# Optimization experiments

Hardware: AMD Instinct MI355X
Metric: run time of the kernel (lower is better)

## Reference

```python
import jax, jax.numpy as jnp
import numpy as np

GROUP_SIZE = 64
NUM_HEADS = 16
NUM_KV_HEADS = 4
ROPE_BASE = 10000.0


def rms_norm(x):
    eps = jnp.asarray(jnp.finfo(x.dtype).eps, x.dtype)
    return x * jax.lax.rsqrt(jnp.mean(x * x, axis=-1, keepdims=True) + eps)


def ternary_weight(w, g=GROUP_SIZE):
    # fake-quant with straight-through estimator, matching torch bf16 cast
    wb = w.astype(jnp.bfloat16)
    wg = wb.reshape(-1, g)
    scale = jnp.clip(jnp.mean(jnp.abs(wg), axis=-1, keepdims=True), 1e-8)
    q = jnp.clip(jnp.round(wg / scale), -1, 1)
    wq = (q * scale).reshape(w.shape)
    return wb + jax.lax.stop_gradient(wq - wb)


def ternary_linear(x, w):
    wt = ternary_weight(w).astype(x.dtype)
    return x @ wt.T


def apply_rotary_emb(x, cos, sin):
    half = x.shape[-1] // 2
    x1, x2 = x[..., :half], x[..., half:]
    return jnp.concatenate((x1 * cos + x2 * sin, x1 * -sin + x2 * cos), axis=-1)


def rotary_tables(seq_len, head_dim, dtype):
    inv_freq = 1.0 / (ROPE_BASE ** (jnp.arange(0, head_dim, 2, dtype=jnp.float32) / head_dim))
    freqs = jnp.outer(jnp.arange(seq_len, dtype=jnp.float32), inv_freq)  # [S, D/2]
    cos = jnp.cos(freqs)[None, :, None, :].astype(dtype)  # [1,S,1,D/2]
    sin = jnp.sin(freqs)[None, :, None, :].astype(dtype)
    return cos, sin


def setup_inputs() -> dict:
    key = jax.random.key(0)
    k1, k2, k3 = jax.random.split(key, 3)
    dim = 1024
    q_size = NUM_HEADS * (dim // NUM_HEADS)
    kv_size = NUM_KV_HEADS * (dim // NUM_HEADS)
    return {
        "x": jax.random.normal(k1, (2, 2048, dim), dtype=jnp.float32),
        "w_qkv": jax.random.normal(k2, (q_size + 2 * kv_size, dim), dtype=jnp.float32) * 0.02,
        "w_proj": jax.random.normal(k3, (dim, dim), dtype=jnp.float32) * 0.02,
        "q_gain": jnp.ones((NUM_HEADS,), dtype=jnp.float32),
    }


def reference(x, w_qkv, w_proj, q_gain):
    bsz, seqlen, dim = x.shape
    head_dim = dim // NUM_HEADS
    q_size = NUM_HEADS * head_dim
    kv_size = NUM_KV_HEADS * head_dim

    qkv = ternary_linear(x, w_qkv)
    q = qkv[..., :q_size].reshape(bsz, seqlen, NUM_HEADS, head_dim)
    k = qkv[..., q_size:q_size + kv_size].reshape(bsz, seqlen, NUM_KV_HEADS, head_dim)
    v = qkv[..., q_size + kv_size:].reshape(bsz, seqlen, NUM_KV_HEADS, head_dim)

    q, k = rms_norm(q), rms_norm(k)
    cos, sin = rotary_tables(seqlen, head_dim, q.dtype)
    q = apply_rotary_emb(q, cos, sin)
    k = apply_rotary_emb(k, cos, sin)
    q = q * q_gain.astype(q.dtype)[None, None, :, None]

    # GQA: repeat kv heads
    rep = NUM_HEADS // NUM_KV_HEADS
    kr = jnp.repeat(k, rep, axis=2)  # [B,S,H,D]
    vr = jnp.repeat(v, rep, axis=2)

    scale = 1.0 / jnp.sqrt(jnp.asarray(head_dim, q.dtype))
    scores = jnp.einsum('bqhd,bkhd->bhqk', q, kr) * scale  # [B,H,S,S]
    causal = jnp.tril(jnp.ones((seqlen, seqlen), dtype=bool))
    scores = jnp.where(causal[None, None], scores, jnp.asarray(-jnp.inf, scores.dtype))
    probs = jax.nn.softmax(scores, axis=-1)
    y = jnp.einsum('bhqk,bkhd->bqhd', probs, vr).reshape(bsz, seqlen, dim)

    # NormedTernaryLinear: rms_norm then ternary linear
    return ternary_linear(rms_norm(y), w_proj)
```

## Files before the change

kernel.cpp:

```cpp
#include <hip/hip_runtime.h>
#include <cstdint>

typedef unsigned short u16;
typedef __bf16 bf16x8 __attribute__((ext_vector_type(8)));
typedef __bf16 bf16x2 __attribute__((ext_vector_type(2)));
typedef short s16x4 __attribute__((ext_vector_type(4)));
typedef int s32x2 __attribute__((ext_vector_type(2)));
typedef float f32x4 __attribute__((ext_vector_type(4)));

__device__ __forceinline__ u16 f2bf(float f) {
    unsigned u = __float_as_uint(f);
    u = (u + 0x7fffu + ((u >> 16) & 1u)) >> 16;
    return (u16)u;
}
__device__ __forceinline__ float bf2f(u16 h) {
    return __uint_as_float(((unsigned)h) << 16);
}

__device__ __forceinline__ void glds16(const u16* g, u16* l) {
    __builtin_amdgcn_global_load_lds(
        (const __attribute__((address_space(1))) void*)g,
        (__attribute__((address_space(3))) void*)l, 16, 0, 0);
}

__device__ __forceinline__ s16x4 pack_bf4(float p0, float p1, float p2, float p3) {
    bf16x2 lo = {(__bf16)p0, (__bf16)p1};
    bf16x2 hi = {(__bf16)p2, (__bf16)p3};
    s32x2 pk = {__builtin_bit_cast(int, lo), __builtin_bit_cast(int, hi)};
    return __builtin_bit_cast(s16x4, pk);
}

#if __has_builtin(__builtin_amdgcn_mfma_f32_16x16x16bf16_1k)
#define MFMA16(a, b, c) __builtin_amdgcn_mfma_f32_16x16x16bf16_1k(a, b, c, 0, 0, 0)
#else
static __device__ __forceinline__ f32x4 mfma16_asm(s16x4 a, s16x4 b, f32x4 c) {
    asm("v_mfma_f32_16x16x16_bf16 %0, %1, %2, %0" : "+v"(c) : "v"(a), "v"(b));
    return c;
}
#define MFMA16(a, b, c) mfma16_asm(a, b, c)
#endif

__global__ __launch_bounds__(256) void prep(
    const float* __restrict__ w_qkv, const float* __restrict__ w_proj,
    const float* __restrict__ x,
    u16* __restrict__ wqkv_b, u16* __restrict__ wproj_b, u16* __restrict__ xb) {
    int bid = blockIdx.x;
    if (bid < 1280) {
        const float* w; u16* o; size_t base;
        if (bid < 768) { w = w_qkv; o = wqkv_b; base = (size_t)bid * 2048; }
        else { w = w_proj; o = wproj_b; base = (size_t)(bid - 768) * 2048; }
        size_t i = base + (size_t)threadIdx.x * 8;
        float4 A = *(const float4*)(w + i);
        float4 B = *(const float4*)(w + i + 4);
        float wf[8] = {A.x, A.y, A.z, A.w, B.x, B.y, B.z, B.w};
        float wbf[8], ab[8];
        #pragma unroll
        for (int e = 0; e < 8; ++e) { wbf[e] = bf2f(f2bf(wf[e])); ab[e] = fabsf(wbf[e]); }
        float s = ((ab[0] + ab[1]) + (ab[2] + ab[3])) + ((ab[4] + ab[5]) + (ab[6] + ab[7]));
        s += __shfl_xor(s, 1);
        s += __shfl_xor(s, 2);
        s += __shfl_xor(s, 4);
        float scale = bf2f(f2bf(s * (1.0f / 64.0f)));
        if (scale < 1e-8f) scale = 1e-8f;
        u16 ov[8];
        #pragma unroll
        for (int e = 0; e < 8; ++e) {
            float t = bf2f(f2bf(wbf[e] / scale));
            float q = rintf(t);
            q = fminf(1.0f, fmaxf(-1.0f, q));
            float d = bf2f(f2bf(q * scale - wbf[e]));
            ov[e] = f2bf(wbf[e] + d);
        }
        *(int4*)(o + i) = *(const int4*)ov;
    } else {
        size_t i = ((size_t)(bid - 1280) * 256 + threadIdx.x) * 8;
        float4 a = *(const float4*)(x + i);
        float4 b = *(const float4*)(x + i + 4);
        u16 o[8] = {f2bf(a.x), f2bf(a.y), f2bf(a.z), f2bf(a.w),
                    f2bf(b.x), f2bf(b.y), f2bf(b.z), f2bf(b.w)};
        *(int4*)(xb + i) = *(const int4*)o;
    }
}

__global__ __launch_bounds__(256) void gemm_qkv(
    const u16* __restrict__ A, const u16* __restrict__ B,
    const float* __restrict__ gain,
    u16* __restrict__ Qb, u16* __restrict__ Kb, u16* __restrict__ Vt) {
    __shared__ u16 As[2][128 * 32];
    __shared__ u16 Bs[2][64 * 32];
    const int tid = threadIdx.x;
    const int lane = tid & 63, w = tid >> 6;
    const int quad = lane >> 4, l16 = lane & 15;
    const int bx = blockIdx.x, by = blockIdx.y;
    const int n0 = bx * 64, t0 = by * 128;
    const bool vblk = bx >= 20;
    const int K = 1024, nk = 32;
    const int b = by >> 4;

    const int sra = w * 16 + (lane >> 2);
    const int srb = tid >> 2;
    const int sg4 = lane & 3;

    f32x4 acc[2][4];
    f32x4 zero = {0.f, 0.f, 0.f, 0.f};
    #pragma unroll
    for (int i = 0; i < 2; ++i)
        #pragma unroll
        for (int j = 0; j < 4; ++j) acc[i][j] = zero;

    int aoff[2], boff[4];
    #pragma unroll
    for (int mi = 0; mi < 2; ++mi) {
        int r = w * 32 + mi * 16 + l16;
        aoff[mi] = r * 32 + (quad ^ ((r >> 1) & 3)) * 8;
    }
    #pragma unroll
    for (int ni = 0; ni < 4; ++ni) {
        int rb = ni * 16 + l16;
        boff[ni] = rb * 32 + (quad ^ ((rb >> 1) & 3)) * 8;
    }

    #pragma unroll
    for (int i = 0; i < 2; ++i) {
        int r = sra + i * 64;
        int g = sg4 ^ ((r >> 1) & 3);
        glds16(A + (size_t)(t0 + r) * K + g * 8, &As[0][0] + (w * 16 + i * 64) * 32 + lane * 8);
    }
    {
        int g = sg4 ^ ((srb >> 1) & 3);
        glds16(B + (size_t)(n0 + srb) * K + g * 8, &Bs[0][0] + w * 512 + lane * 8);
    }
    __syncthreads();

    for (int kt = 0; kt < nk; ++kt) {
        if (kt + 1 < nk) {
            int k0 = (kt + 1) * 32, bi = (kt + 1) & 1;
            #pragma unroll
            for (int i = 0; i < 2; ++i) {
                int r = sra + i * 64;
                int g = sg4 ^ ((r >> 1) & 3);
                glds16(A + (size_t)(t0 + r) * K + k0 + g * 8, &As[bi][0] + (w * 16 + i * 64) * 32 + lane * 8);
            }
            int g = sg4 ^ ((srb >> 1) & 3);
            glds16(B + (size_t)(n0 + srb) * K + k0 + g * 8, &Bs[bi][0] + w * 512 + lane * 8);
        }
        const u16* as = &As[kt & 1][0];
        const u16* bs = &Bs[kt & 1][0];
        bf16x8 af[2], bfr[4];
        #pragma unroll
        for (int mi = 0; mi < 2; ++mi) af[mi]  = *(const bf16x8*)(as + aoff[mi]);
        #pragma unroll
        for (int ni = 0; ni < 4; ++ni) bfr[ni] = *(const bf16x8*)(bs + boff[ni]);
        if (!vblk) {
            #pragma unroll
            for (int mi = 0; mi < 2; ++mi)
                #pragma unroll
                for (int ni = 0; ni < 4; ++ni)
                    acc[mi][ni] = __builtin_amdgcn_mfma_f32_16x16x32_bf16(af[mi], bfr[ni], acc[mi][ni], 0, 0, 0);
        } else {
            #pragma unroll
            for (int mi = 0; mi < 2; ++mi)
                #pragma unroll
                for (int ni = 0; ni < 4; ++ni)
                    acc[mi][ni] = __builtin_amdgcn_mfma_f32_16x16x32_bf16(bfr[ni], af[mi], acc[mi][ni], 0, 0, 0);
        }
        __syncthreads();
    }

    if (vblk) {
        const int kv = bx - 20;
        u16* vbase = Vt + (size_t)(b * 4 + kv) * 64 * 2048;
        const int si = (t0 + w * 32 + l16) & 2047;
        #pragma unroll
        for (int mi = 0; mi < 2; ++mi)
            #pragma unroll
            for (int ni = 0; ni < 4; ++ni) {
                int d = ni * 16 + quad * 4;
                #pragma unroll
                for (int r = 0; r < 4; ++r)
                    vbase[(size_t)(d + r) * 2048 + si + mi * 16] = f2bf(acc[mi][ni][r]);
            }
    } else {
        const bool isQ = bx < 16;
        const float sc = 0.18033688011112042f;
        const float g = isQ ? gain[bx] * sc : 1.0f;
        u16* base = isQ ? (Qb + (size_t)(b * 16 + bx) * 2048 * 64)
                        : (Kb + (size_t)(b * 4 + (bx - 16)) * 2048 * 64);
        const float eps = 1.1920929e-7f;
        const float invf0 = (float)(1.0 / pow(10000.0, (double)l16 / 32.0));
        const float invf1 = (float)(1.0 / pow(10000.0, (double)(l16 + 16) / 32.0));
        #pragma unroll
        for (int mi = 0; mi < 2; ++mi) {
            #pragma unroll
            for (int r = 0; r < 4; ++r) {
                float v0 = acc[mi][0][r], v1 = acc[mi][1][r];
                float v2 = acc[mi][2][r], v3 = acc[mi][3][r];
                float ssq = (v0 * v0 + v1 * v1) + (v2 * v2 + v3 * v3);
                #pragma unroll
                for (int m = 1; m < 16; m <<= 1) ssq += __shfl_xor(ssq, m);
                float rn = 1.0f / sqrtf(ssq * (1.0f / 64.0f) + eps);
                int si = (t0 + w * 32 + mi * 16 + quad * 4 + r) & 2047;
                float a0 = (float)si * invf0, a1 = (float)si * invf1;
                float c0 = __cosf(a0), s0 = __sinf(a0);
                float c1 = __cosf(a1), s1 = __sinf(a1);
                float x1a = v0 * rn, x2a = v2 * rn;
                float x1b = v1 * rn, x2b = v3 * rn;
                u16* row = base + (size_t)si * 64;
                row[l16]      = f2bf((x1a * c0 + x2a * s0) * g);
                row[l16 + 32] = f2bf((x2a * c0 - x1a * s0) * g);
                row[l16 + 16] = f2bf((x1b * c1 + x2b * s1) * g);
                row[l16 + 48] = f2bf((x2b * c1 - x1b * s1) * g);
            }
        }
    }
}

__global__ __launch_bounds__(256) void gemm_bt(
    const u16* __restrict__ A, const u16* __restrict__ B,
    float* __restrict__ C, int M, int N, int K) {
    __shared__ u16 As[2][128 * 32];
    __shared__ u16 Bs[2][64 * 32];
    const int tid = threadIdx.x;
    const int lane = tid & 63, w = tid >> 6;
    const int quad = lane >> 4, l16 = lane & 15;
    const int m0 = blockIdx.y * 128, n0 = blockIdx.x * 64;
    const int wm = (w >> 1) * 64, wn = (w & 1) * 32;

    const int sra = w * 16 + (lane >> 2);
    const int srb = tid >> 2;
    const int sg4 = lane & 3;

    f32x4 acc[4][2];
    f32x4 zero = {0.f, 0.f, 0.f, 0.f};
    #pragma unroll
    for (int i = 0; i < 4; ++i) { acc[i][0] = zero; acc[i][1] = zero; }

    int aoff[4], boff[2];
    #pragma unroll
    for (int mi = 0; mi < 4; ++mi) {
        int r = wm + mi * 16 + l16;
        aoff[mi] = r * 32 + (quad ^ ((r >> 1) & 3)) * 8;
    }
    #pragma unroll
    for (int ni = 0; ni < 2; ++ni) {
        int r = wn + ni * 16 + l16;
        boff[ni] = r * 32 + (quad ^ ((r >> 1) & 3)) * 8;
    }

    const int nk = K >> 5;
    #pragma unroll
    for (int i = 0; i < 2; ++i) {
        int r = sra + i * 64;
        int g = sg4 ^ ((r >> 1) & 3);
        glds16(A + (size_t)(m0 + r) * K + g * 8, &As[0][0] + (w * 16 + i * 64) * 32 + lane * 8);
    }
    {
        int g = sg4 ^ ((srb >> 1) & 3);
        glds16(B + (size_t)(n0 + srb) * K + g * 8, &Bs[0][0] + w * 512 + lane * 8);
    }
    __syncthreads();

    for (int kt = 0; kt < nk; ++kt) {
        if (kt + 1 < nk) {
            int k0 = (kt + 1) * 32, bi = (kt + 1) & 1;
            #pragma unroll
            for (int i = 0; i < 2; ++i) {
                int r = sra + i * 64;
                int g = sg4 ^ ((r >> 1) & 3);
                glds16(A + (size_t)(m0 + r) * K + k0 + g * 8, &As[bi][0] + (w * 16 + i * 64) * 32 + lane * 8);
            }
            int g = sg4 ^ ((srb >> 1) & 3);
            glds16(B + (size_t)(n0 + srb) * K + k0 + g * 8, &Bs[bi][0] + w * 512 + lane * 8);
        }
        const u16* as = &As[kt & 1][0];
        const u16* bs = &Bs[kt & 1][0];
        bf16x8 af[4], bfr[2];
        #pragma unroll
        for (int mi = 0; mi < 4; ++mi) af[mi]  = *(const bf16x8*)(as + aoff[mi]);
        #pragma unroll
        for (int ni = 0; ni < 2; ++ni) bfr[ni] = *(const bf16x8*)(bs + boff[ni]);
        #pragma unroll
        for (int mi = 0; mi < 4; ++mi)
            #pragma unroll
            for (int ni = 0; ni < 2; ++ni)
                acc[mi][ni] = __builtin_amdgcn_mfma_f32_16x16x32_bf16(af[mi], bfr[ni], acc[mi][ni], 0, 0, 0);
        __syncthreads();
    }
    #pragma unroll
    for (int mi = 0; mi < 4; ++mi)
        #pragma unroll
        for (int ni = 0; ni < 2; ++ni) {
            int rg = m0 + wm + mi * 16 + quad * 4;
            int cg = n0 + wn + ni * 16 + l16;
            float* cp = C + (size_t)rg * N + cg;
            #pragma unroll
            for (int r = 0; r < 4; ++r) cp[(size_t)r * N] = acc[mi][ni][r];
        }
}

__global__ __launch_bounds__(512, 4) void attn(
    const u16* __restrict__ Qb, const u16* __restrict__ Kb,
    const u16* __restrict__ Vt, const float* __restrict__ gain,
    float* __restrict__ y, float* __restrict__ Opart, float* __restrict__ ml) {
    __shared__ u16 Ks[2][64 * 64];
    __shared__ u16 Vsh[2][64 * 64];
    const int hb = blockIdx.x;
    const int h = hb & 15, b = hb >> 4, kvh = h >> 2;
    const int yid = blockIdx.y;
    int bq, c0, nj, sb = 0; bool partial;
    if (yid < 5) {
        bq = yid; c0 = 0; nj = 2 * bq + 2; partial = false;
    } else if (yid < 17) {
        int t = yid - 5; bq = 5 + (t >> 1); int ch = t & 1, T = 2 * bq + 2;
        c0 = (ch * T) >> 1; nj = (((ch + 1) * T) >> 1) - c0; partial = true;
        sb = (bq - 5) * 2 + ch;
    } else {
        int t = yid - 17; bq = 11 + t / 3; int ch = t - (t / 3) * 3, T = 2 * bq + 2;
        c0 = ch * T / 3; nj = (ch + 1) * T / 3 - c0; partial = true;
        sb = 12 + (bq - 11) * 3 + ch;
    }
    const int q0 = bq * 128;
    const int tid = threadIdx.x, lane = tid & 63, w = tid >> 6;
    const int quad = lane >> 4, l16 = lane & 15;
    const float nM = -(12.0f * fabsf(gain[h]) + 1.0f);
    const f32x4 minit = {nM, nM, nM, nM};

    const u16* Qg = Qb + ((size_t)(b * 16 + h) * 2048 + q0) * 64;
    const u16* Kg = Kb + (size_t)(b * 4 + kvh) * 2048 * 64;
    const u16* Vg = Vt + (size_t)(b * 4 + kvh) * 64 * 2048;

    const bf16x8 qa0 = *(const bf16x8*)(Qg + (size_t)(w * 16 + l16) * 64 + quad * 8);
    const bf16x8 qa1 = *(const bf16x8*)(Qg + (size_t)(w * 16 + l16) * 64 + 32 + quad * 8);

    const int sr = tid >> 3;
    const int sg = (tid & 7) ^ (sr & 7);
    u16* kd[2] = {&Ks[0][0] + tid * 8, &Ks[1][0] + tid * 8};
    u16* vd[2] = {&Vsh[0][0] + tid * 8, &Vsh[1][0] + tid * 8};

    {
        int c = (c0 + nj - 1) * 64;
        glds16(Kg + (size_t)(c + sr) * 64 + sg * 8, kd[(nj - 1) & 1]);
        glds16(Vg + (size_t)sr * 2048 + c + sg * 8, vd[(nj - 1) & 1]);
    }
    __syncthreads();

    f32x4 o[4];
    f32x4 zero = {0.f, 0.f, 0.f, 0.f};
    #pragma unroll
    for (int t = 0; t < 4; ++t) o[t] = zero;
    float l = 0.f;

    for (int jj = nj - 1; jj >= 0; --jj) {
        if (jj > 0) {
            int c = (c0 + jj - 1) * 64;
            glds16(Kg + (size_t)(c + sr) * 64 + sg * 8, kd[(jj - 1) & 1]);
            glds16(Vg + (size_t)sr * 2048 + c + sg * 8, vd[(jj - 1) & 1]);
        }
        const u16* Kt = (jj & 1) ? &Ks[1][0] : &Ks[0][0];
        const u16* Vl = (jj & 1) ? &Vsh[1][0] : &Vsh[0][0];
        const int d = 8 * bq + w - 4 * (c0 + jj);
        if (d >= 0) {
            const int tmax = d < 3 ? d : 3;
            f32x4 st[4];
            __builtin_amdgcn_s_setprio(1);
            #pragma unroll
            for (int t = 0; t < 4; ++t) {
                if (t <= tmax) {
                    int rk = t * 16 + l16;
                    bf16x8 kb0 = *(const bf16x8*)(Kt + rk * 64 + ((quad ^ (rk & 7)) * 8));
                    bf16x8 kb1 = *(const bf16x8*)(Kt + rk * 64 + (((quad + 4) ^ (rk & 7)) * 8));
                    f32x4 s = __builtin_amdgcn_mfma_f32_16x16x32_bf16(kb0, qa0, minit, 0, 0, 0);
                    s = __builtin_amdgcn_mfma_f32_16x16x32_bf16(kb1, qa1, s, 0, 0, 0);
                    if (t == d) {
                        #pragma unroll
                        for (int r = 0; r < 4; ++r)
                            if (quad * 4 + r > l16) s[r] = -1e30f;
                    }
                    st[t] = s;
                }
            }
            __builtin_amdgcn_s_setprio(0);
            float rs = 0.f;
            s16x4 pf[4];
            #pragma unroll
            for (int t = 0; t < 4; ++t) {
                if (t <= tmax) {
                    float p0 = __builtin_amdgcn_exp2f(st[t][0]);
                    float p1 = __builtin_amdgcn_exp2f(st[t][1]);
                    float p2 = __builtin_amdgcn_exp2f(st[t][2]);
                    float p3 = __builtin_amdgcn_exp2f(st[t][3]);
                    rs += (p0 + p1) + (p2 + p3);
                    pf[t] = pack_bf4(p0, p1, p2, p3);
                }
            }
            l += rs;
            __builtin_amdgcn_s_setprio(1);
            #pragma unroll
            for (int dt = 0; dt < 4; ++dt) {
                int rv = dt * 16 + l16;
                #pragma unroll
                for (int kt = 0; kt < 4; ++kt) {
                    if (kt <= tmax) {
                        int gv = 2 * kt + (quad >> 1);
                        s16x4 va = *(const s16x4*)(Vl + rv * 64 + ((gv ^ (rv & 7)) * 8) + (quad & 1) * 4);
                        o[dt] = MFMA16(va, pf[kt], o[dt]);
                    }
                }
            }
            __builtin_amdgcn_s_setprio(0);
        }
        __syncthreads();
    }

    l += __shfl_xor(l, 16);
    l += __shfl_xor(l, 32);

    const int q = w * 16 + l16;
    if (!partial) {
        const float inv = 1.0f / l;
        const size_t row = (size_t)b * 2048 + q0 + q;
        #pragma unroll
        for (int dt = 0; dt < 4; ++dt) {
            f32x4 a = o[dt] * inv;
            *(f32x4*)(&y[row * 1024 + h * 64 + dt * 16 + quad * 4]) = a;
        }
    } else {
        const int slot = hb * 27 + sb;
        float* Op = Opart + (size_t)slot * 8192;
        #pragma unroll
        for (int dt = 0; dt < 4; ++dt)
            *(f32x4*)(Op + q * 64 + dt * 16 + quad * 4) = o[dt];
        if (quad == 0) ml[slot * 128 + q] = l;
    }
}

__global__ __launch_bounds__(256) void rmsnorm_merge(
    const float* __restrict__ y, const float* __restrict__ Opart,
    const float* __restrict__ ml, u16* __restrict__ yb) {
    __shared__ float red[4];
    const int row = blockIdx.x, tid = threadIdx.x;
    const int b = row >> 11, s = row & 2047;
    float4 v;
    if (s < 640) {
        v = *(const float4*)(y + (size_t)row * 1024 + tid * 4);
    } else {
        const int bq = s >> 7, q = s & 127;
        const int e = tid * 4, h = e >> 6, dh = e & 63;
        const int ns = bq < 11 ? 2 : 3;
        const int sb = bq < 11 ? (bq - 5) * 2 : 12 + (bq - 11) * 3;
        const int slot = (b * 16 + h) * 27 + sb;
        float l = ml[slot * 128 + q] + ml[(slot + 1) * 128 + q];
        const float* P0 = Opart + (size_t)slot * 8192 + q * 64 + dh;
        f32x4 x = *(const f32x4*)P0 + *(const f32x4*)(P0 + 8192);
        if (ns == 3) {
            l += ml[(slot + 2) * 128 + q];
            x += *(const f32x4*)(P0 + 16384);
        }
        float inv = 1.0f / l;
        v.x = x[0] * inv; v.y = x[1] * inv; v.z = x[2] * inv; v.w = x[3] * inv;
    }
    float ss = v.x * v.x + v.y * v.y + v.z * v.z + v.w * v.w;
    #pragma unroll
    for (int m = 1; m < 64; m <<= 1) ss += __shfl_xor(ss, m);
    if ((tid & 63) == 0) red[tid >> 6] = ss;
    __syncthreads();
    float tot = red[0] + red[1] + red[2] + red[3];
    float rn = 1.0f / sqrtf(tot * (1.0f / 1024.0f) + 1.1920929e-7f);
    u16 o[4] = {f2bf(v.x * rn), f2bf(v.y * rn), f2bf(v.z * rn), f2bf(v.w * rn)};
    *(uint2*)(yb + (size_t)row * 1024 + tid * 4) = *(const uint2*)o;
}

extern "C" void kernel_launch(void* const* d_in, const int* in_sizes, int n_in,
                              void* d_out, int out_size, void* d_ws, size_t ws_size,
                              hipStream_t stream) {
    const float* x      = (const float*)d_in[0];
    const float* w_qkv  = (const float*)d_in[1];
    const float* w_proj = (const float*)d_in[2];
    const float* q_gain = (const float*)d_in[3];
    float* out = (float*)d_out;
    char* ws = (char*)d_ws;

    u16*   wproj_b = (u16*)(ws);
    u16*   xb      = (u16*)(ws + 2097152);
    float* y       = (float*)(ws + 2097152);
    u16*   wqkv_b  = (u16*)(ws + 10485760);
    u16*   Qb      = (u16*)(ws + 18874368);
    u16*   yb      = (u16*)(ws + 18874368);
    u16*   Kb      = (u16*)(ws + 27262976);
    u16*   Vt      = (u16*)(ws + 29360128);
    float* Opart   = (float*)(ws + 31457280);
    float* mlb     = (float*)(ws + 59768832);

    prep<<<3328, 256, 0, stream>>>(w_qkv, w_proj, x, wqkv_b, wproj_b, xb);
    gemm_qkv<<<dim3(24, 32), 256, 0, stream>>>(xb, wqkv_b, q_gain, Qb, Kb, Vt);
    attn<<<dim3(32, 32), 512, 0, stream>>>(Qb, Kb, Vt, q_gain, y, Opart, mlb);
    rmsnorm_merge<<<4096, 256, 0, stream>>>(y, Opart, mlb, yb);
    gemm_bt<<<dim3(16, 32), 256, 0, stream>>>(yb, wproj_b, out, 4096, 1024, 1024);
}
```

Baseline: 181.5 us.

## Triple-buffer LDS tiles with vmcnt waits and one barrier per iteration

```diff
diff --git a/kernel.cpp b/kernel.cpp
--- a/kernel.cpp
+++ b/kernel.cpp
@@ -7,6 +7,8 @@
 typedef short s16x4 __attribute__((ext_vector_type(4)));
 typedef int s32x2 __attribute__((ext_vector_type(2)));
 typedef float f32x4 __attribute__((ext_vector_type(4)));
+
+#define WAITVM(n) asm volatile("s_waitcnt vmcnt(" #n ")" ::: "memory")
 
 __device__ __forceinline__ u16 f2bf(float f) {
     unsigned u = __float_as_uint(f);
@@ -86,8 +88,8 @@
     const u16* __restrict__ A, const u16* __restrict__ B,
     const float* __restrict__ gain,
     u16* __restrict__ Qb, u16* __restrict__ Kb, u16* __restrict__ Vt) {
-    __shared__ u16 As[2][128 * 32];
-    __shared__ u16 Bs[2][64 * 32];
+    __shared__ u16 As[3 * 4096];
+    __shared__ u16 Bs[3 * 2048];
     const int tid = threadIdx.x;
     const int lane = tid & 63, w = tid >> 6;
     const int quad = lane >> 4, l16 = lane & 15;
@@ -100,6 +102,8 @@
     const int sra = w * 16 + (lane >> 2);
     const int srb = tid >> 2;
     const int sg4 = lane & 3;
+    const int adst = (w * 16) * 32 + lane * 8;
+    const int bdst = w * 512 + lane * 8;
 
     f32x4 acc[2][4];
     f32x4 zero = {0.f, 0.f, 0.f, 0.f};
@@ -124,28 +128,34 @@
     for (int i = 0; i < 2; ++i) {
         int r = sra + i * 64;
         int g = sg4 ^ ((r >> 1) & 3);
-        glds16(A + (size_t)(t0 + r) * K + g * 8, &As[0][0] + (w * 16 + i * 64) * 32 + lane * 8);
+        glds16(A + (size_t)(t0 + r) * K + g * 8, As + adst + i * 2048);
     }
     {
         int g = sg4 ^ ((srb >> 1) & 3);
-        glds16(B + (size_t)(n0 + srb) * K + g * 8, &Bs[0][0] + w * 512 + lane * 8);
-    }
-    __syncthreads();
-
+        glds16(B + (size_t)(n0 + srb) * K + g * 8, Bs + bdst);
+    }
+
+    int cb = 0;
     for (int kt = 0; kt < nk; ++kt) {
+        int pb = cb == 2 ? 0 : cb + 1;
         if (kt + 1 < nk) {
-            int k0 = (kt + 1) * 32, bi = (kt + 1) & 1;
+            int k0 = (kt + 1) * 32;
             #pragma unroll
             for (int i = 0; i < 2; ++i) {
                 int r = sra + i * 64;
                 int g = sg4 ^ ((r >> 1) & 3);
-                glds16(A + (size_t)(t0 + r) * K + k0 + g * 8, &As[bi][0] + (w * 16 + i * 64) * 32 + lane * 8);
+                glds16(A + (size_t)(t0 + r) * K + k0 + g * 8, As + pb * 4096 + adst + i * 2048);
             }
             int g = sg4 ^ ((srb >> 1) & 3);
-            glds16(B + (size_t)(n0 + srb) * K + k0 + g * 8, &Bs[bi][0] + w * 512 + lane * 8);
-        }
-        const u16* as = &As[kt & 1][0];
-        const u16* bs = &Bs[kt & 1][0];
+            glds16(B + (size_t)(n0 + srb) * K + k0 + g * 8, Bs + pb * 2048 + bdst);
+            WAITVM(3);
+        } else {
+            WAITVM(0);
+        }
+        __builtin_amdgcn_s_barrier();
+        __builtin_amdgcn_sched_barrier(0);
+        const u16* as = As + cb * 4096;
+        const u16* bs = Bs + cb * 2048;
         bf16x8 af[2], bfr[4];
         #pragma unroll
         for (int mi = 0; mi < 2; ++mi) af[mi]  = *(const bf16x8*)(as + aoff[mi]);
@@ -164,7 +174,7 @@
                 for (int ni = 0; ni < 4; ++ni)
                     acc[mi][ni] = __builtin_amdgcn_mfma_f32_16x16x32_bf16(bfr[ni], af[mi], acc[mi][ni], 0, 0, 0);
         }
-        __syncthreads();
+        cb = pb;
     }
 
     if (vblk) {
@@ -218,8 +228,8 @@
 __global__ __launch_bounds__(256) void gemm_bt(
     const u16* __restrict__ A, const u16* __restrict__ B,
     float* __restrict__ C, int M, int N, int K) {
-    __shared__ u16 As[2][128 * 32];
-    __shared__ u16 Bs[2][64 * 32];
+    __shared__ u16 As[3 * 4096];
+    __shared__ u16 Bs[3 * 2048];
     const int tid = threadIdx.x;
     const int lane = tid & 63, w = tid >> 6;
     const int quad = lane >> 4, l16 = lane & 15;
@@ -229,6 +239,8 @@
     const int sra = w * 16 + (lane >> 2);
     const int srb = tid >> 2;
     const int sg4 = lane & 3;
+    const int adst = (w * 16) * 32 + lane * 8;
+    const int bdst = w * 512 + lane * 8;
 
     f32x4 acc[4][2];
     f32x4 zero = {0.f, 0.f, 0.f, 0.f};
@@ -252,28 +264,34 @@
     for (int i = 0; i < 2; ++i) {
         int r = sra + i * 64;
         int g = sg4 ^ ((r >> 1) & 3);
-        glds16(A + (size_t)(m0 + r) * K + g * 8, &As[0][0] + (w * 16 + i * 64) * 32 + lane * 8);
+        glds16(A + (size_t)(m0 + r) * K + g * 8, As + adst + i * 2048);
     }
     {
         int g = sg4 ^ ((srb >> 1) & 3);
-        glds16(B + (size_t)(n0 + srb) * K + g * 8, &Bs[0][0] + w * 512 + lane * 8);
-    }
-    __syncthreads();
-
+        glds16(B + (size_t)(n0 + srb) * K + g * 8, Bs + bdst);
+    }
+
+    int cb = 0;
     for (int kt = 0; kt < nk; ++kt) {
+        int pb = cb == 2 ? 0 : cb + 1;
         if (kt + 1 < nk) {
-            int k0 = (kt + 1) * 32, bi = (kt + 1) & 1;
+            int k0 = (kt + 1) * 32;
             #pragma unroll
             for (int i = 0; i < 2; ++i) {
                 int r = sra + i * 64;
                 int g = sg4 ^ ((r >> 1) & 3);
-                glds16(A + (size_t)(m0 + r) * K + k0 + g * 8, &As[bi][0] + (w * 16 + i * 64) * 32 + lane * 8);
+                glds16(A + (size_t)(m0 + r) * K + k0 + g * 8, As + pb * 4096 + adst + i * 2048);
             }
             int g = sg4 ^ ((srb >> 1) & 3);
-            glds16(B + (size_t)(n0 + srb) * K + k0 + g * 8, &Bs[bi][0] + w * 512 + lane * 8);
-        }
-        const u16* as = &As[kt & 1][0];
-        const u16* bs = &Bs[kt & 1][0];
+            glds16(B + (size_t)(n0 + srb) * K + k0 + g * 8, Bs + pb * 2048 + bdst);
+            WAITVM(3);
+        } else {
+            WAITVM(0);
+        }
+        __builtin_amdgcn_s_barrier();
+        __builtin_amdgcn_sched_barrier(0);
+        const u16* as = As + cb * 4096;
+        const u16* bs = Bs + cb * 2048;
         bf16x8 af[4], bfr[2];
         #pragma unroll
         for (int mi = 0; mi < 4; ++mi) af[mi]  = *(const bf16x8*)(as + aoff[mi]);
@@ -284,7 +302,7 @@
             #pragma unroll
             for (int ni = 0; ni < 2; ++ni)
                 acc[mi][ni] = __builtin_amdgcn_mfma_f32_16x16x32_bf16(af[mi], bfr[ni], acc[mi][ni], 0, 0, 0);
-        __syncthreads();
+        cb = pb;
     }
     #pragma unroll
     for (int mi = 0; mi < 4; ++mi)
@@ -302,8 +320,8 @@
     const u16* __restrict__ Qb, const u16* __restrict__ Kb,
     const u16* __restrict__ Vt, const float* __restrict__ gain,
     float* __restrict__ y, float* __restrict__ Opart, float* __restrict__ ml) {
-    __shared__ u16 Ks[2][64 * 64];
-    __shared__ u16 Vsh[2][64 * 64];
+    __shared__ u16 KsA[3 * 4096];
+    __shared__ u16 VsA[3 * 4096];
     const int hb = blockIdx.x;
     const int h = hb & 15, b = hb >> 4, kvh = h >> 2;
     const int yid = blockIdx.y;
@@ -334,15 +352,14 @@
 
     const int sr = tid >> 3;
     const int sg = (tid & 7) ^ (sr & 7);
-    u16* kd[2] = {&Ks[0][0] + tid * 8, &Ks[1][0] + tid * 8};
-    u16* vd[2] = {&Vsh[0][0] + tid * 8, &Vsh[1][0] + tid * 8};
-
+    const int so = tid * 8;
+
+    int cb = (nj - 1) % 3;
     {
         int c = (c0 + nj - 1) * 64;
-        glds16(Kg + (size_t)(c + sr) * 64 + sg * 8, kd[(nj - 1) & 1]);
-        glds16(Vg + (size_t)sr * 2048 + c + sg * 8, vd[(nj - 1) & 1]);
-    }
-    __syncthreads();
+        glds16(Kg + (size_t)(c + sr) * 64 + sg * 8, KsA + cb * 4096 + so);
+        glds16(Vg + (size_t)sr * 2048 + c + sg * 8, VsA + cb * 4096 + so);
+    }
 
     f32x4 o[4];
     f32x4 zero = {0.f, 0.f, 0.f, 0.f};
@@ -351,13 +368,19 @@
     float l = 0.f;
 
     for (int jj = nj - 1; jj >= 0; --jj) {
+        int pb = cb ? cb - 1 : 2;
         if (jj > 0) {
             int c = (c0 + jj - 1) * 64;
-            glds16(Kg + (size_t)(c + sr) * 64 + sg * 8, kd[(jj - 1) & 1]);
-            glds16(Vg + (size_t)sr * 2048 + c + sg * 8, vd[(jj - 1) & 1]);
-        }
-        const u16* Kt = (jj & 1) ? &Ks[1][0] : &Ks[0][0];
-        const u16* Vl = (jj & 1) ? &Vsh[1][0] : &Vsh[0][0];
+            glds16(Kg + (size_t)(c + sr) * 64 + sg * 8, KsA + pb * 4096 + so);
+            glds16(Vg + (size_t)sr * 2048 + c + sg * 8, VsA + pb * 4096 + so);
+            WAITVM(2);
+        } else {
+            WAITVM(0);
+        }
+        __builtin_amdgcn_s_barrier();
+        __builtin_amdgcn_sched_barrier(0);
+        const u16* Kt = KsA + cb * 4096;
+        const u16* Vl = VsA + cb * 4096;
         const int d = 8 * bq + w - 4 * (c0 + jj);
         if (d >= 0) {
             const int tmax = d < 3 ? d : 3;
@@ -409,7 +432,7 @@
             }
             __builtin_amdgcn_s_setprio(0);
         }
-        __syncthreads();
+        cb = pb;
     }
 
     l += __shfl_xor(l, 16);
```

Result: no change. 181.9 us (+0.2%).

## Process two query tiles per wave and split KV work more finely

Applied to the files above, without the earlier changes.

```diff
diff --git a/kernel.cpp b/kernel.cpp
--- a/kernel.cpp
+++ b/kernel.cpp
@@ -298,28 +298,27 @@
         }
 }
 
-__global__ __launch_bounds__(512, 4) void attn(
+__global__ __launch_bounds__(256, 4) void attn(
     const u16* __restrict__ Qb, const u16* __restrict__ Kb,
     const u16* __restrict__ Vt, const float* __restrict__ gain,
     float* __restrict__ y, float* __restrict__ Opart, float* __restrict__ ml) {
-    __shared__ u16 Ks[2][64 * 64];
-    __shared__ u16 Vsh[2][64 * 64];
+    __shared__ u16 Ks[2][4096];
+    __shared__ u16 Vs[2][4096];
     const int hb = blockIdx.x;
     const int h = hb & 15, b = hb >> 4, kvh = h >> 2;
     const int yid = blockIdx.y;
-    int bq, c0, nj, sb = 0; bool partial;
-    if (yid < 5) {
-        bq = yid; c0 = 0; nj = 2 * bq + 2; partial = false;
-    } else if (yid < 17) {
-        int t = yid - 5; bq = 5 + (t >> 1); int ch = t & 1, T = 2 * bq + 2;
-        c0 = (ch * T) >> 1; nj = (((ch + 1) * T) >> 1) - c0; partial = true;
-        sb = (bq - 5) * 2 + ch;
-    } else {
-        int t = yid - 17; bq = 11 + t / 3; int ch = t - (t / 3) * 3, T = 2 * bq + 2;
-        c0 = ch * T / 3; nj = (ch + 1) * T / 3 - c0; partial = true;
-        sb = 12 + (bq - 11) * 3 + ch;
-    }
+    const int nch_t[16] = {1,1,2,2,2,3,3,4,4,4,5,5,6,6,6,7};
+    const int cst_t[16] = {0,1,2,4,6,8,11,14,18,22,26,31,36,42,48,54};
+    int bq = 0;
+    #pragma unroll
+    for (int i = 1; i < 16; ++i) if (yid >= cst_t[i]) bq = i;
+    const int nc = nch_t[bq], ch = yid - cst_t[bq];
+    const int T = 2 * bq + 2;
+    const int c0 = ch * T / nc;
+    const int nj = (ch + 1) * T / nc - c0;
+    const bool partial = nc > 1;
     const int q0 = bq * 128;
+
     const int tid = threadIdx.x, lane = tid & 63, w = tid >> 6;
     const int quad = lane >> 4, l16 = lane & 15;
     const float nM = -(12.0f * fabsf(gain[h]) + 1.0f);
@@ -329,81 +328,99 @@
     const u16* Kg = Kb + (size_t)(b * 4 + kvh) * 2048 * 64;
     const u16* Vg = Vt + (size_t)(b * 4 + kvh) * 64 * 2048;
 
-    const bf16x8 qa0 = *(const bf16x8*)(Qg + (size_t)(w * 16 + l16) * 64 + quad * 8);
-    const bf16x8 qa1 = *(const bf16x8*)(Qg + (size_t)(w * 16 + l16) * 64 + 32 + quad * 8);
+    const int qr0 = w * 32 + l16;
+    const bf16x8 qa00 = *(const bf16x8*)(Qg + (size_t)qr0 * 64 + quad * 8);
+    const bf16x8 qa01 = *(const bf16x8*)(Qg + (size_t)qr0 * 64 + 32 + quad * 8);
+    const bf16x8 qa10 = *(const bf16x8*)(Qg + (size_t)(qr0 + 16) * 64 + quad * 8);
+    const bf16x8 qa11 = *(const bf16x8*)(Qg + (size_t)(qr0 + 16) * 64 + 32 + quad * 8);
 
     const int sr = tid >> 3;
     const int sg = (tid & 7) ^ (sr & 7);
-    u16* kd[2] = {&Ks[0][0] + tid * 8, &Ks[1][0] + tid * 8};
-    u16* vd[2] = {&Vsh[0][0] + tid * 8, &Vsh[1][0] + tid * 8};
+    const int so = tid * 8;
 
     {
-        int c = (c0 + nj - 1) * 64;
-        glds16(Kg + (size_t)(c + sr) * 64 + sg * 8, kd[(nj - 1) & 1]);
-        glds16(Vg + (size_t)sr * 2048 + c + sg * 8, vd[(nj - 1) & 1]);
+        int c = (c0 + nj - 1) * 64, bi = (nj - 1) & 1;
+        glds16(Kg + (size_t)(c + sr) * 64 + sg * 8,        &Ks[bi][0] + so);
+        glds16(Kg + (size_t)(c + sr + 32) * 64 + sg * 8,   &Ks[bi][0] + so + 2048);
+        glds16(Vg + (size_t)sr * 2048 + c + sg * 8,        &Vs[bi][0] + so);
+        glds16(Vg + (size_t)(sr + 32) * 2048 + c + sg * 8, &Vs[bi][0] + so + 2048);
     }
     __syncthreads();
 
-    f32x4 o[4];
+    f32x4 o0[4], o1[4];
     f32x4 zero = {0.f, 0.f, 0.f, 0.f};
     #pragma unroll
-    for (int t = 0; t < 4; ++t) o[t] = zero;
-    float l = 0.f;
+    for (int t = 0; t < 4; ++t) { o0[t] = zero; o1[t] = zero; }
+    float l0 = 0.f, l1 = 0.f;
 
     for (int jj = nj - 1; jj >= 0; --jj) {
         if (jj > 0) {
-            int c = (c0 + jj - 1) * 64;
-            glds16(Kg + (size_t)(c + sr) * 64 + sg * 8, kd[(jj - 1) & 1]);
-            glds16(Vg + (size_t)sr * 2048 + c + sg * 8, vd[(jj - 1) & 1]);
-        }
-        const u16* Kt = (jj & 1) ? &Ks[1][0] : &Ks[0][0];
-        const u16* Vl = (jj & 1) ? &Vsh[1][0] : &Vsh[0][0];
-        const int d = 8 * bq + w - 4 * (c0 + jj);
-        if (d >= 0) {
-            const int tmax = d < 3 ? d : 3;
-            f32x4 st[4];
+            int c = (c0 + jj - 1) * 64, bi = (jj - 1) & 1;
+            glds16(Kg + (size_t)(c + sr) * 64 + sg * 8,        &Ks[bi][0] + so);
+            glds16(Kg + (size_t)(c + sr + 32) * 64 + sg * 8,   &Ks[bi][0] + so + 2048);
+            glds16(Vg + (size_t)sr * 2048 + c + sg * 8,        &Vs[bi][0] + so);
+            glds16(Vg + (size_t)(sr + 32) * 2048 + c + sg * 8, &Vs[bi][0] + so + 2048);
+        }
+        const u16* Kt = &Ks[jj & 1][0];
+        const u16* Vl = &Vs[jj & 1][0];
+        const int jg = c0 + jj;
+        const int d0 = 8 * bq + 2 * w - 4 * jg;
+        const int d1 = d0 + 1;
+        if (d1 >= 0) {
+            const int tm0 = d0 < 3 ? d0 : 3;
+            const int tm1 = d1 < 3 ? d1 : 3;
+            s16x4 pf0[4], pf1[4];
+            float rs0 = 0.f, rs1 = 0.f;
             __builtin_amdgcn_s_setprio(1);
             #pragma unroll
             for (int t = 0; t < 4; ++t) {
-                if (t <= tmax) {
+                if (t <= tm1) {
                     int rk = t * 16 + l16;
                     bf16x8 kb0 = *(const bf16x8*)(Kt + rk * 64 + ((quad ^ (rk & 7)) * 8));
                     bf16x8 kb1 = *(const bf16x8*)(Kt + rk * 64 + (((quad + 4) ^ (rk & 7)) * 8));
-                    f32x4 s = __builtin_amdgcn_mfma_f32_16x16x32_bf16(kb0, qa0, minit, 0, 0, 0);
-                    s = __builtin_amdgcn_mfma_f32_16x16x32_bf16(kb1, qa1, s, 0, 0, 0);
-                    if (t == d) {
-                        #pragma unroll
-                        for (int r = 0; r < 4; ++r)
-                            if (quad * 4 + r > l16) s[r] = -1e30f;
+                    if (t <= tm0) {
+                        f32x4 s = __builtin_amdgcn_mfma_f32_16x16x32_bf16(kb0, qa00, minit, 0, 0, 0);
+                        s = __builtin_amdgcn_mfma_f32_16x16x32_bf16(kb1, qa01, s, 0, 0, 0);
+                        if (t == d0) {
+                            #pragma unroll
+                            for (int r = 0; r < 4; ++r)
+                                if (quad * 4 + r > l16) s[r] = -1e30f;
+                        }
+                        float p0 = __builtin_amdgcn_exp2f(s[0]);
+                        float p1 = __builtin_amdgcn_exp2f(s[1]);
+                        float p2 = __builtin_amdgcn_exp2f(s[2]);
+                        float p3 = __builtin_amdgcn_exp2f(s[3]);
+                        rs0 += (p0 + p1) + (p2 + p3);
+                        pf0[t] = pack_bf4(p0, p1, p2, p3);
                     }
-                    st[t] = s;
+                    {
+                        f32x4 s = __builtin_amdgcn_mfma_f32_16x16x32_bf16(kb0, qa10, minit, 0, 0, 0);
+                        s = __builtin_amdgcn_mfma_f32_16x16x32_bf16(kb1, qa11, s, 0, 0, 0);
+                        if (t == d1) {
+                            #pragma unroll
+                            for (int r = 0; r < 4; ++r)
+                                if (quad * 4 + r > l16) s[r] = -1e30f;
+                        }
+                        float p0 = __builtin_amdgcn_exp2f(s[0]);
+                        float p1 = __builtin_amdgcn_exp2f(s[1]);
+                        float p2 = __builtin_amdgcn_exp2f(s[2]);
+                        float p3 = __builtin_amdgcn_exp2f(s[3]);
+                        rs1 += (p0 + p1) + (p2 + p3);
+                        pf1[t] = pack_bf4(p0, p1, p2, p3);
+                    }
                 }
             }
-            __builtin_amdgcn_s_setprio(0);
-            float rs = 0.f;
-            s16x4 pf[4];
-            #pragma unroll
-            for (int t = 0; t < 4; ++t) {
-                if (t <= tmax) {
-                    float p0 = __builtin_amdgcn_exp2f(st[t][0]);
-                    float p1 = __builtin_amdgcn_exp2f(st[t][1]);
-                    float p2 = __builtin_amdgcn_exp2f(st[t][2]);
-                    float p3 = __builtin_amdgcn_exp2f(st[t][3]);
-                    rs += (p0 + p1) + (p2 + p3);
-                    pf[t] = pack_bf4(p0, p1, p2, p3);
-                }
-            }
-            l += rs;
-            __builtin_amdgcn_s_setprio(1);
+            l0 += rs0; l1 += rs1;
             #pragma unroll
             for (int dt = 0; dt < 4; ++dt) {
                 int rv = dt * 16 + l16;
                 #pragma unroll
                 for (int kt = 0; kt < 4; ++kt) {
-                    if (kt <= tmax) {
+                    if (kt <= tm1) {
                         int gv = 2 * kt + (quad >> 1);
                         s16x4 va = *(const s16x4*)(Vl + rv * 64 + ((gv ^ (rv & 7)) * 8) + (quad & 1) * 4);
-                        o[dt] = MFMA16(va, pf[kt], o[dt]);
+                        if (kt <= tm0) o0[dt] = MFMA16(va, pf0[kt], o0[dt]);
+                        o1[dt] = MFMA16(va, pf1[kt], o1[dt]);
                     }
                 }
             }
@@ -412,25 +429,34 @@
         __syncthreads();
     }
 
-    l += __shfl_xor(l, 16);
-    l += __shfl_xor(l, 32);
-
-    const int q = w * 16 + l16;
+    l0 += __shfl_xor(l0, 16);
+    l0 += __shfl_xor(l0, 32);
+    l1 += __shfl_xor(l1, 16);
+    l1 += __shfl_xor(l1, 32);
+
+    const int q = w * 32 + l16;
     if (!partial) {
-        const float inv = 1.0f / l;
-        const size_t row = (size_t)b * 2048 + q0 + q;
+        const float inv0 = 1.0f / l0, inv1 = 1.0f / l1;
+        const size_t row0 = (size_t)b * 2048 + q0 + q;
         #pragma unroll
         for (int dt = 0; dt < 4; ++dt) {
-            f32x4 a = o[dt] * inv;
-            *(f32x4*)(&y[row * 1024 + h * 64 + dt * 16 + quad * 4]) = a;
+            f32x4 a = o0[dt] * inv0;
+            *(f32x4*)(&y[row0 * 1024 + h * 64 + dt * 16 + quad * 4]) = a;
+            f32x4 c = o1[dt] * inv1;
+            *(f32x4*)(&y[(row0 + 16) * 1024 + h * 64 + dt * 16 + quad * 4]) = c;
         }
     } else {
-        const int slot = hb * 27 + sb;
+        const int slot = hb * 59 + (yid - 2);
         float* Op = Opart + (size_t)slot * 8192;
         #pragma unroll
-        for (int dt = 0; dt < 4; ++dt)
-            *(f32x4*)(Op + q * 64 + dt * 16 + quad * 4) = o[dt];
-        if (quad == 0) ml[slot * 128 + q] = l;
+        for (int dt = 0; dt < 4; ++dt) {
+            *(f32x4*)(Op + q * 64 + dt * 16 + quad * 4) = o0[dt];
+            *(f32x4*)(Op + (q + 16) * 64 + dt * 16 + quad * 4) = o1[dt];
+        }
+        if (quad == 0) {
+            ml[slot * 128 + q] = l0;
+            ml[slot * 128 + q + 16] = l1;
+        }
     }
 }
 
@@ -441,23 +467,24 @@
     const int row = blockIdx.x, tid = threadIdx.x;
     const int b = row >> 11, s = row & 2047;
     float4 v;
-    if (s < 640) {
+    if (s < 256) {
         v = *(const float4*)(y + (size_t)row * 1024 + tid * 4);
     } else {
+        const int nch_t[16] = {1,1,2,2,2,3,3,4,4,4,5,5,6,6,6,7};
+        const int cst_t[16] = {0,1,2,4,6,8,11,14,18,22,26,31,36,42,48,54};
         const int bq = s >> 7, q = s & 127;
         const int e = tid * 4, h = e >> 6, dh = e & 63;
-        const int ns = bq < 11 ? 2 : 3;
-        const int sb = bq < 11 ? (bq - 5) * 2 : 12 + (bq - 11) * 3;
-        const int slot = (b * 16 + h) * 27 + sb;
-        float l = ml[slot * 128 + q] + ml[(slot + 1) * 128 + q];
-        const float* P0 = Opart + (size_t)slot * 8192 + q * 64 + dh;
-        f32x4 x = *(const f32x4*)P0 + *(const f32x4*)(P0 + 8192);
-        if (ns == 3) {
-            l += ml[(slot + 2) * 128 + q];
-            x += *(const f32x4*)(P0 + 16384);
+        const int n = nch_t[bq];
+        const int slot0 = (b * 16 + h) * 59 + (cst_t[bq] - 2);
+        float l = 0.f;
+        f32x4 xa = {0.f, 0.f, 0.f, 0.f};
+        const float* P = Opart + (size_t)slot0 * 8192 + q * 64 + dh;
+        for (int c = 0; c < n; ++c) {
+            l += ml[(size_t)(slot0 + c) * 128 + q];
+            xa += *(const f32x4*)(P + (size_t)c * 8192);
         }
         float inv = 1.0f / l;
-        v.x = x[0] * inv; v.y = x[1] * inv; v.z = x[2] * inv; v.w = x[3] * inv;
+        v.x = xa[0] * inv; v.y = xa[1] * inv; v.z = xa[2] * inv; v.w = xa[3] * inv;
     }
     float ss = v.x * v.x + v.y * v.y + v.z * v.z + v.w * v.w;
     #pragma unroll
@@ -489,11 +516,11 @@
     u16*   Kb      = (u16*)(ws + 27262976);
     u16*   Vt      = (u16*)(ws + 29360128);
     float* Opart   = (float*)(ws + 31457280);
-    float* mlb     = (float*)(ws + 59768832);
+    float* mlb     = (float*)(ws + 93323264);
 
     prep<<<3328, 256, 0, stream>>>(w_qkv, w_proj, x, wqkv_b, wproj_b, xb);
     gemm_qkv<<<dim3(24, 32), 256, 0, stream>>>(xb, wqkv_b, q_gain, Qb, Kb, Vt);
-    attn<<<dim3(32, 32), 512, 0, stream>>>(Qb, Kb, Vt, q_gain, y, Opart, mlb);
+    attn<<<dim3(32, 61), 256, 0, stream>>>(Qb, Kb, Vt, q_gain, y, Opart, mlb);
     rmsnorm_merge<<<4096, 256, 0, stream>>>(y, Opart, mlb, yb);
     gemm_bt<<<dim3(16, 32), 256, 0, stream>>>(yb, wproj_b, out, 4096, 1024, 1024);
 }
```

After: 177.1 us. 1.03x faster.
